# Optimization experiments

Hardware: AMD Instinct MI355X
Metric: run time of the kernel (lower is better)

The kernel has to match this reference:

```python
import jax, jax.numpy as jnp
import numpy as np

CHUNK = 512  # tile size along N; keeps per-step [B,CHUNK,M] tile ~64 MB, never builds full [B,N,M]


def setup_inputs() -> dict:
    key = jax.random.key(0)
    k1, k2 = jax.random.split(key)
    xyz1 = jax.random.normal(k1, (4, 8192, 3), dtype=jnp.float32)
    xyz2 = jax.random.normal(k2, (4, 8192, 3), dtype=jnp.float32)
    return {"xyz1": xyz1, "xyz2": xyz2}


def _chamfer(xyz1, xyz2):
    # xyz1: [B,N,3], xyz2: [B,M,3]
    B, N, _ = xyz1.shape
    M = xyz2.shape[1]
    K = N // CHUNK
    x1_chunks = xyz1.reshape(B, K, CHUNK, 3).transpose(1, 0, 2, 3)  # [K,B,C,3]

    def step(carry, x1k):
        best_d2, best_i2, start = carry  # running mins for xyz2 -> xyz1 direction
        # squared distances for this tile: [B,C,M]
        d = jnp.sum((x1k[:, :, None, :] - xyz2[:, None, :, :]) ** 2, axis=-1)
        # xyz1 -> xyz2: min over M
        d1 = jnp.min(d, axis=2)                              # [B,C]
        i1 = jnp.argmin(d, axis=2).astype(jnp.int32)         # [B,C]
        # xyz2 -> xyz1: partial min over this chunk of N
        dc = jnp.min(d, axis=1)                              # [B,M]
        ic = jnp.argmin(d, axis=1).astype(jnp.int32) + start # [B,M], global index
        upd = dc < best_d2
        best_d2 = jnp.where(upd, dc, best_d2)
        best_i2 = jnp.where(upd, ic, best_i2)
        return (best_d2, best_i2, start + CHUNK), (d1, i1)

    init = (jnp.full((B, M), jnp.inf, dtype=xyz1.dtype),
            jnp.zeros((B, M), dtype=jnp.int32),
            jnp.int32(0))
    (dist2, idx2, _), (d1s, i1s) = jax.lax.scan(step, init, x1_chunks)
    dist1 = d1s.transpose(1, 0, 2).reshape(B, N)
    idx1 = i1s.transpose(1, 0, 2).reshape(B, N)
    return dist1, dist2, idx1, idx2


def reference(xyz1, xyz2):
    # Matches ChamferDistance.forward: (dist1, dist2, idx1, idx2),
    # squared nearest-neighbor distances and int32 argmin indices.
    return _chamfer(xyz1, xyz2)
```

## Files before the change

### kernel.cpp

```cpp
#include <hip/hip_runtime.h>
#include <math.h>


#define QPT 4
#define BLK 256
#define QPB (QPT*BLK)

__global__ __launch_bounds__(256, 4) void chamfer_main(
    const float* __restrict__ xyz1, const float* __restrict__ xyz2,
    unsigned long long* __restrict__ pp,
    int N, int M, int B, int S, int C)
{
    const int dir = blockIdx.z;
    const float* q = dir ? xyz2 : xyz1;
    const float* r = dir ? xyz1 : xyz2;
    const int Nq = dir ? M : N;
    const int Nr = dir ? N : M;
    const int b     = blockIdx.y / S;
    const int split = blockIdx.y % S;
    const int base  = split * C;

    extern __shared__ float s[];

    {
        const float4* gv = (const float4*)(r + ((size_t)b * Nr + base) * 3);
        float4* sv = (float4*)s;
        const int elems4 = C * 3 / 4;
        for (int t = threadIdx.x; t < elems4; t += BLK) sv[t] = gv[t];
    }
    __syncthreads();

    float qx[QPT], qy[QPT], qz[QPT];
    int qi[QPT];
    bool qv[QPT];
#pragma unroll
    for (int k = 0; k < QPT; ++k) {
        qi[k] = blockIdx.x * QPB + k * BLK + threadIdx.x;
        qv[k] = qi[k] < Nq;
        const float* qp = q + ((size_t)b * Nq + (qv[k] ? qi[k] : 0)) * 3;
        qx[k] = qp[0]; qy[k] = qp[1]; qz[k] = qp[2];
    }

    float bd[QPT];
    int   gi[QPT];
#pragma unroll
    for (int k = 0; k < QPT; ++k) { bd[k] = INFINITY; gi[k] = 0; }

    const float4* sv = (const float4*)s;
    const int iters = C / 8;
    for (int j8 = 0; j8 < iters; ++j8) {
        float4 f0 = sv[6 * j8 + 0];
        float4 f1 = sv[6 * j8 + 1];
        float4 f2 = sv[6 * j8 + 2];
        float4 f3 = sv[6 * j8 + 3];
        float4 f4 = sv[6 * j8 + 4];
        float4 f5 = sv[6 * j8 + 5];
        float px[8] = { f0.x, f0.w, f1.z, f2.y, f3.x, f3.w, f4.z, f5.y };
        float py[8] = { f0.y, f1.x, f1.w, f2.z, f3.y, f4.x, f4.w, f5.z };
        float pz[8] = { f0.z, f1.y, f2.x, f2.w, f3.z, f4.y, f5.x, f5.w };
#pragma unroll
        for (int k = 0; k < QPT; ++k) {
            float d[8];
#pragma unroll
            for (int p = 0; p < 8; ++p) {
                float dx = qx[k] - px[p];
                float dy = qy[k] - py[p];
                float dz = qz[k] - pz[p];
                d[p] = fmaf(dx, dx, fmaf(dy, dy, dz * dz));
            }
            float m01 = fminf(d[0], d[1]);
            float m23 = fminf(d[2], d[3]);
            float m45 = fminf(d[4], d[5]);
            float m67 = fminf(d[6], d[7]);
            float m = fminf(fminf(m01, m23), fminf(m45, m67));
            if (m < bd[k]) { bd[k] = m; gi[k] = j8; }
        }
    }

    const size_t obase = (size_t)(dir * B + b) * Nq;
#pragma unroll
    for (int k = 0; k < QPT; ++k) {
        if (!qv[k]) continue;
        const int g = gi[k];
        float4 f0 = sv[6 * g + 0];
        float4 f1 = sv[6 * g + 1];
        float4 f2 = sv[6 * g + 2];
        float4 f3 = sv[6 * g + 3];
        float4 f4 = sv[6 * g + 4];
        float4 f5 = sv[6 * g + 5];
        float px[8] = { f0.x, f0.w, f1.z, f2.y, f3.x, f3.w, f4.z, f5.y };
        float py[8] = { f0.y, f1.x, f1.w, f2.z, f3.y, f4.x, f4.w, f5.z };
        float pz[8] = { f0.z, f1.y, f2.x, f2.w, f3.z, f4.y, f5.x, f5.w };
        int best = 0;
#pragma unroll
        for (int p = 7; p >= 0; --p) {
            float dx = qx[k] - px[p];
            float dy = qy[k] - py[p];
            float dz = qz[k] - pz[p];
            float d = fmaf(dx, dx, fmaf(dy, dy, dz * dz));
            if (d == bd[k]) best = p;
        }
        const int idx = base + g * 8 + best;
        unsigned long long packed =
            ((unsigned long long)__float_as_uint(bd[k]) << 32) | (unsigned)idx;
        atomicMin(&pp[obase + qi[k]], packed);
    }
}

__global__ __launch_bounds__(256) void chamfer_final(
    const unsigned long long* __restrict__ pp,
    float* __restrict__ out, int N, int M, int B)
{
    const int gid = blockIdx.x * blockDim.x + threadIdx.x;
    const int perDir0 = B * N;
    int dir, rem;
    if (gid < perDir0) { dir = 0; rem = gid; }
    else if (gid < perDir0 + B * M) { dir = 1; rem = gid - perDir0; }
    else return;
    const int Nq = dir ? M : N;

    unsigned long long v = pp[(size_t)(dir * B) * Nq + rem];

    float* dist_out = out + (dir ? (size_t)B * N : 0);
    float* idx_out  = out + (size_t)B * N + (size_t)B * M + (dir ? (size_t)B * N : 0);
    dist_out[rem] = __uint_as_float((unsigned)(v >> 32));
    idx_out[rem]  = (float)(unsigned)(v & 0xffffffffu);
}

extern "C" void kernel_launch(void* const* d_in, const int* in_sizes, int n_in,
                              void* d_out, int out_size, void* d_ws, size_t ws_size,
                              hipStream_t stream) {
    const float* xyz1 = (const float*)d_in[0];
    const float* xyz2 = (const float*)d_in[1];
    float* out = (float*)d_out;
    const int B = 4;
    const int N = in_sizes[0] / (B * 3);
    const int M = in_sizes[1] / (B * 3);
    const int NQ = (N > M ? N : M);
    const int NR = (N > M ? N : M);

    int S = 32;
    while (NR % (S * 8)) S >>= 1;
    const int C = NR / S;

    unsigned long long* pp = (unsigned long long*)d_ws;
    const int nslots = 2 * B * NQ;

    hipMemsetAsync(pp, 0xFF, (size_t)nslots * 8, stream);

    dim3 grid((NQ + QPB - 1) / QPB, B * S, 2);
    size_t lds = (size_t)C * 3 * sizeof(float);
    chamfer_main<<<grid, dim3(BLK, 1, 1), lds, stream>>>(
        xyz1, xyz2, pp, N, M, B, S, C);

    chamfer_final<<<dim3((nslots + 255) / 256, 1, 1), dim3(256, 1, 1), 0, stream>>>(
        pp, out, N, M, B);
}
```

Measured before the change: 125.5 us.

## Use expanded-norm distance form in inner loop with near-tie exact fallback

Replaces the direct (q-p)^2 distance in the hot loop with |p|^2 - 2q·p, where the per-point norm is computed once per reference group and shared across all queries, giving three FMAs per pair instead of subtract-and-square. Because this surrogate loses precision, the loop also tracks a second-best group minimum. When the top two groups fall within an epsilon, an exact brute-force rescan over the shared-memory chunk is run; otherwise the winning group is rescored exactly. This adds register pressure and a rare divergent slow path, and correctness now depends on the epsilon being large enough to cover rounding differences.

```diff
diff --git a/kernel.cpp b/kernel.cpp
--- a/kernel.cpp
+++ b/kernel.cpp
@@ -31,6 +31,7 @@
     __syncthreads();
 
     float qx[QPT], qy[QPT], qz[QPT];
+    float n2x[QPT], n2y[QPT], n2z[QPT];
     int qi[QPT];
     bool qv[QPT];
 #pragma unroll
@@ -39,12 +40,13 @@
         qv[k] = qi[k] < Nq;
         const float* qp = q + ((size_t)b * Nq + (qv[k] ? qi[k] : 0)) * 3;
         qx[k] = qp[0]; qy[k] = qp[1]; qz[k] = qp[2];
+        n2x[k] = -2.0f * qx[k]; n2y[k] = -2.0f * qy[k]; n2z[k] = -2.0f * qz[k];
     }
 
-    float bd[QPT];
+    float bd[QPT], bd2[QPT];
     int   gi[QPT];
 #pragma unroll
-    for (int k = 0; k < QPT; ++k) { bd[k] = INFINITY; gi[k] = 0; }
+    for (int k = 0; k < QPT; ++k) { bd[k] = INFINITY; bd2[k] = INFINITY; gi[k] = 0; }
 
     const float4* sv = (const float4*)s;
     const int iters = C / 8;
@@ -58,8 +60,61 @@
         float px[8] = { f0.x, f0.w, f1.z, f2.y, f3.x, f3.w, f4.z, f5.y };
         float py[8] = { f0.y, f1.x, f1.w, f2.z, f3.y, f4.x, f4.w, f5.z };
         float pz[8] = { f0.z, f1.y, f2.x, f2.w, f3.z, f4.y, f5.x, f5.w };
+        float u[8];
+#pragma unroll
+        for (int p = 0; p < 8; ++p)
+            u[p] = fmaf(pz[p], pz[p], fmaf(py[p], py[p], px[p] * px[p]));
 #pragma unroll
         for (int k = 0; k < QPT; ++k) {
+            float ma = INFINITY, mb = INFINITY;
+#pragma unroll
+            for (int p = 0; p < 8; p += 2) {
+                float ta = fmaf(n2x[k], px[p],
+                           fmaf(n2y[k], py[p],
+                           fmaf(n2z[k], pz[p], u[p])));
+                float tb = fmaf(n2x[k], px[p + 1],
+                           fmaf(n2y[k], py[p + 1],
+                           fmaf(n2z[k], pz[p + 1], u[p + 1])));
+                ma = fminf(ma, ta);
+                mb = fminf(mb, tb);
+            }
+            float m = fminf(ma, mb);
+            float old = bd[k];
+            bool c = m < old;
+            bd[k]  = c ? m : old;
+            gi[k]  = c ? j8 : gi[k];
+            bd2[k] = fminf(bd2[k], fmaxf(old, m));
+        }
+    }
+
+    const size_t obase = (size_t)(dir * B + b) * Nq;
+    const float eps = 2e-5f;
+#pragma unroll
+    for (int k = 0; k < QPT; ++k) {
+        if (!qv[k]) continue;
+        unsigned long long packed;
+        if (bd2[k] - bd[k] < eps) {
+            float best = INFINITY; int bidx = 0;
+            for (int j = 0; j < C; ++j) {
+                float dx = qx[k] - s[3 * j + 0];
+                float dy = qy[k] - s[3 * j + 1];
+                float dz = qz[k] - s[3 * j + 2];
+                float d = fmaf(dx, dx, fmaf(dy, dy, dz * dz));
+                if (d < best) { best = d; bidx = j; }
+            }
+            packed = ((unsigned long long)__float_as_uint(best) << 32)
+                   | (unsigned)(base + bidx);
+        } else {
+            const int g = gi[k];
+            float4 f0 = sv[6 * g + 0];
+            float4 f1 = sv[6 * g + 1];
+            float4 f2 = sv[6 * g + 2];
+            float4 f3 = sv[6 * g + 3];
+            float4 f4 = sv[6 * g + 4];
+            float4 f5 = sv[6 * g + 5];
+            float px[8] = { f0.x, f0.w, f1.z, f2.y, f3.x, f3.w, f4.z, f5.y };
+            float py[8] = { f0.y, f1.x, f1.w, f2.z, f3.y, f4.x, f4.w, f5.z };
+            float pz[8] = { f0.z, f1.y, f2.x, f2.w, f3.z, f4.y, f5.x, f5.w };
             float d[8];
 #pragma unroll
             for (int p = 0; p < 8; ++p) {
@@ -68,41 +123,15 @@
                 float dz = qz[k] - pz[p];
                 d[p] = fmaf(dx, dx, fmaf(dy, dy, dz * dz));
             }
-            float m01 = fminf(d[0], d[1]);
-            float m23 = fminf(d[2], d[3]);
-            float m45 = fminf(d[4], d[5]);
-            float m67 = fminf(d[6], d[7]);
-            float m = fminf(fminf(m01, m23), fminf(m45, m67));
-            if (m < bd[k]) { bd[k] = m; gi[k] = j8; }
+            float m = fminf(fminf(fminf(d[0], d[1]), fminf(d[2], d[3])),
+                            fminf(fminf(d[4], d[5]), fminf(d[6], d[7])));
+            int best = 0;
+#pragma unroll
+            for (int p = 7; p >= 0; --p)
+                if (d[p] == m) best = p;
+            packed = ((unsigned long long)__float_as_uint(m) << 32)
+                   | (unsigned)(base + g * 8 + best);
         }
-    }
-
-    const size_t obase = (size_t)(dir * B + b) * Nq;
-#pragma unroll
-    for (int k = 0; k < QPT; ++k) {
-        if (!qv[k]) continue;
-        const int g = gi[k];
-        float4 f0 = sv[6 * g + 0];
-        float4 f1 = sv[6 * g + 1];
-        float4 f2 = sv[6 * g + 2];
-        float4 f3 = sv[6 * g + 3];
-        float4 f4 = sv[6 * g + 4];
-        float4 f5 = sv[6 * g + 5];
-        float px[8] = { f0.x, f0.w, f1.z, f2.y, f3.x, f3.w, f4.z, f5.y };
-        float py[8] = { f0.y, f1.x, f1.w, f2.z, f3.y, f4.x, f4.w, f5.z };
-        float pz[8] = { f0.z, f1.y, f2.x, f2.w, f3.z, f4.y, f5.x, f5.w };
-        int best = 0;
-#pragma unroll
-        for (int p = 7; p >= 0; --p) {
-            float dx = qx[k] - px[p];
-            float dy = qy[k] - py[p];
-            float dz = qz[k] - pz[p];
-            float d = fmaf(dx, dx, fmaf(dy, dy, dz * dz));
-            if (d == bd[k]) best = p;
-        }
-        const int idx = base + g * 8 + best;
-        unsigned long long packed =
-            ((unsigned long long)__float_as_uint(bd[k]) << 32) | (unsigned)idx;
         atomicMin(&pp[obase + qi[k]], packed);
     }
 }
```

Result: slower. 130.0 us (+3.6%).

## Transpose LDS tile to SoA and use packed float2 math for distances

Applied to the files above, without the earlier changes.

Stores the reference tile in shared memory as separate x/y/z arrays (SoA) instead of interleaved xyz, so each component can be loaded as contiguous float4s. The distance computation is rewritten with two-wide float vectors so the compiler can emit packed FP32 instructions (v_pk_fma/v_pk_add) and halve the ALU instruction count in the hot loop. The global-to-LDS copy becomes scalar with a divide-by-3 per element and scattered LDS writes, adding cost to the staging phase.

```diff
diff --git a/kernel.cpp b/kernel.cpp
--- a/kernel.cpp
+++ b/kernel.cpp
@@ -5,6 +5,8 @@
 #define QPT 4
 #define BLK 256
 #define QPB (QPT*BLK)
+
+typedef float v2f __attribute__((ext_vector_type(2)));
 
 __global__ __launch_bounds__(256, 4) void chamfer_main(
     const float* __restrict__ xyz1, const float* __restrict__ xyz2,
@@ -23,14 +25,16 @@
     extern __shared__ float s[];
 
     {
-        const float4* gv = (const float4*)(r + ((size_t)b * Nr + base) * 3);
-        float4* sv = (float4*)s;
-        const int elems4 = C * 3 / 4;
-        for (int t = threadIdx.x; t < elems4; t += BLK) sv[t] = gv[t];
+        const float* g = r + ((size_t)b * Nr + base) * 3;
+        for (int t = threadIdx.x; t < 3 * C; t += BLK) {
+            float v = g[t];
+            int pt = t / 3, comp = t - 3 * pt;
+            s[comp * C + pt] = v;
+        }
     }
     __syncthreads();
 
-    float qx[QPT], qy[QPT], qz[QPT];
+    v2f qxv[QPT], qyv[QPT], qzv[QPT];
     int qi[QPT];
     bool qv[QPT];
 #pragma unroll
@@ -38,7 +42,9 @@
         qi[k] = blockIdx.x * QPB + k * BLK + threadIdx.x;
         qv[k] = qi[k] < Nq;
         const float* qp = q + ((size_t)b * Nq + (qv[k] ? qi[k] : 0)) * 3;
-        qx[k] = qp[0]; qy[k] = qp[1]; qz[k] = qp[2];
+        qxv[k] = (v2f){qp[0], qp[0]};
+        qyv[k] = (v2f){qp[1], qp[1]};
+        qzv[k] = (v2f){qp[2], qp[2]};
     }
 
     float bd[QPT];
@@ -46,33 +52,32 @@
 #pragma unroll
     for (int k = 0; k < QPT; ++k) { bd[k] = INFINITY; gi[k] = 0; }
 
-    const float4* sv = (const float4*)s;
+    const float4* svx = (const float4*)(s);
+    const float4* svy = (const float4*)(s + C);
+    const float4* svz = (const float4*)(s + 2 * C);
     const int iters = C / 8;
     for (int j8 = 0; j8 < iters; ++j8) {
-        float4 f0 = sv[6 * j8 + 0];
-        float4 f1 = sv[6 * j8 + 1];
-        float4 f2 = sv[6 * j8 + 2];
-        float4 f3 = sv[6 * j8 + 3];
-        float4 f4 = sv[6 * j8 + 4];
-        float4 f5 = sv[6 * j8 + 5];
-        float px[8] = { f0.x, f0.w, f1.z, f2.y, f3.x, f3.w, f4.z, f5.y };
-        float py[8] = { f0.y, f1.x, f1.w, f2.z, f3.y, f4.x, f4.w, f5.z };
-        float pz[8] = { f0.z, f1.y, f2.x, f2.w, f3.z, f4.y, f5.x, f5.w };
+        float4 X0 = svx[2 * j8 + 0], X1 = svx[2 * j8 + 1];
+        float4 Y0 = svy[2 * j8 + 0], Y1 = svy[2 * j8 + 1];
+        float4 Z0 = svz[2 * j8 + 0], Z1 = svz[2 * j8 + 1];
+        v2f xp[4] = { {X0.x, X0.y}, {X0.z, X0.w}, {X1.x, X1.y}, {X1.z, X1.w} };
+        v2f yp[4] = { {Y0.x, Y0.y}, {Y0.z, Y0.w}, {Y1.x, Y1.y}, {Y1.z, Y1.w} };
+        v2f zp[4] = { {Z0.x, Z0.y}, {Z0.z, Z0.w}, {Z1.x, Z1.y}, {Z1.z, Z1.w} };
 #pragma unroll
         for (int k = 0; k < QPT; ++k) {
-            float d[8];
+            v2f d2[4];
 #pragma unroll
-            for (int p = 0; p < 8; ++p) {
-                float dx = qx[k] - px[p];
-                float dy = qy[k] - py[p];
-                float dz = qz[k] - pz[p];
-                d[p] = fmaf(dx, dx, fmaf(dy, dy, dz * dz));
+            for (int i = 0; i < 4; ++i) {
+                v2f dx = qxv[k] - xp[i];
+                v2f dy = qyv[k] - yp[i];
+                v2f dz = qzv[k] - zp[i];
+                d2[i] = __builtin_elementwise_fma(
+                            dx, dx, __builtin_elementwise_fma(dy, dy, dz * dz));
             }
-            float m01 = fminf(d[0], d[1]);
-            float m23 = fminf(d[2], d[3]);
-            float m45 = fminf(d[4], d[5]);
-            float m67 = fminf(d[6], d[7]);
-            float m = fminf(fminf(m01, m23), fminf(m45, m67));
+            v2f e0 = __builtin_elementwise_min(d2[0], d2[1]);
+            v2f e1 = __builtin_elementwise_min(d2[2], d2[3]);
+            v2f e  = __builtin_elementwise_min(e0, e1);
+            float m = fminf(e.x, e.y);
             if (m < bd[k]) { bd[k] = m; gi[k] = j8; }
         }
     }
@@ -82,21 +87,19 @@
     for (int k = 0; k < QPT; ++k) {
         if (!qv[k]) continue;
         const int g = gi[k];
-        float4 f0 = sv[6 * g + 0];
-        float4 f1 = sv[6 * g + 1];
-        float4 f2 = sv[6 * g + 2];
-        float4 f3 = sv[6 * g + 3];
-        float4 f4 = sv[6 * g + 4];
-        float4 f5 = sv[6 * g + 5];
-        float px[8] = { f0.x, f0.w, f1.z, f2.y, f3.x, f3.w, f4.z, f5.y };
-        float py[8] = { f0.y, f1.x, f1.w, f2.z, f3.y, f4.x, f4.w, f5.z };
-        float pz[8] = { f0.z, f1.y, f2.x, f2.w, f3.z, f4.y, f5.x, f5.w };
+        float4 X0 = svx[2 * g + 0], X1 = svx[2 * g + 1];
+        float4 Y0 = svy[2 * g + 0], Y1 = svy[2 * g + 1];
+        float4 Z0 = svz[2 * g + 0], Z1 = svz[2 * g + 1];
+        float xs[8] = { X0.x, X0.y, X0.z, X0.w, X1.x, X1.y, X1.z, X1.w };
+        float ys[8] = { Y0.x, Y0.y, Y0.z, Y0.w, Y1.x, Y1.y, Y1.z, Y1.w };
+        float zs[8] = { Z0.x, Z0.y, Z0.z, Z0.w, Z1.x, Z1.y, Z1.z, Z1.w };
+        const float qx = qxv[k].x, qy = qyv[k].x, qz = qzv[k].x;
         int best = 0;
 #pragma unroll
         for (int p = 7; p >= 0; --p) {
-            float dx = qx[k] - px[p];
-            float dy = qy[k] - py[p];
-            float dz = qz[k] - pz[p];
+            float dx = qx - xs[p];
+            float dy = qy - ys[p];
+            float dz = qz - zs[p];
             float d = fmaf(dx, dx, fmaf(dy, dy, dz * dz));
             if (d == bd[k]) best = p;
         }
```

Result: no change. 125.6 us (+0.1%).
